# Optimization experiments

Hardware: AMD Instinct MI355X
Metric: run time of the kernel (lower is better)

Reference implementation:

```python
import jax, jax.numpy as jnp
import numpy as np

N, E, D = 50000, 300000, 64
EPS = 0.0  # eps buffer, train_eps=False


def setup_inputs() -> dict:
    key = jax.random.key(0)
    ks = jax.random.split(key, 24)
    inp = {}
    i = 0
    for d in range(3):
        inp[f"x{d}"] = jax.random.normal(ks[i], (N, D), jnp.float32); i += 1
        inp[f"up_index{d}"] = jax.random.randint(ks[i], (2, E), 0, N, jnp.int32); i += 1
        inp[f"down_index{d}"] = jax.random.randint(ks[i], (2, E), 0, N, jnp.int32); i += 1
        inp[f"up_attr{d}"] = jax.random.normal(ks[i], (E, D), jnp.float32); i += 1
        inp[f"down_attr{d}"] = jax.random.normal(ks[i], (E, D), jnp.float32); i += 1
    s2 = 1.0 / np.sqrt(2 * D)
    s1 = 1.0 / np.sqrt(D)
    inp["W_up"] = jax.random.normal(ks[i], (2 * D, D), jnp.float32) * s2; i += 1
    inp["b_up"] = jnp.zeros((D,), jnp.float32)
    inp["W_down"] = jax.random.normal(ks[i], (2 * D, D), jnp.float32) * s2; i += 1
    inp["b_down"] = jnp.zeros((D,), jnp.float32)
    inp["W1"] = jax.random.normal(ks[i], (D, D), jnp.float32) * s1; i += 1
    inp["b1"] = jnp.zeros((D,), jnp.float32)
    inp["W2"] = jax.random.normal(ks[i], (D, D), jnp.float32) * s1; i += 1
    inp["b2"] = jnp.zeros((D,), jnp.float32)
    return inp


def _level(x, up_idx, down_idx, up_attr, down_attr,
           W_up, b_up, W_down, b_down, W1, b1, W2, b2):
    # message_up: gather source feats, concat attr, MLP, scatter-add to targets
    m_up = jax.nn.relu(jnp.concatenate([x[up_idx[1]], up_attr], axis=-1) @ W_up + b_up)
    out_up = jax.ops.segment_sum(m_up, up_idx[0], num_segments=N)
    m_dn = jax.nn.relu(jnp.concatenate([x[down_idx[1]], down_attr], axis=-1) @ W_down + b_down)
    out_dn = jax.ops.segment_sum(m_dn, down_idx[0], num_segments=N)
    # out_up += (1+eps)x; out_down += (1+eps)x; update(out_up + out_down)
    h = out_up + out_dn + (2.0 * (1.0 + EPS)) * x
    return jax.nn.relu(jax.nn.relu(h @ W1 + b1) @ W2 + b2)


def reference(x0, up_index0, down_index0, up_attr0, down_attr0,
              x1, up_index1, down_index1, up_attr1, down_attr1,
              x2, up_index2, down_index2, up_attr2, down_attr2,
              W_up, b_up, W_down, b_down, W1, b1, W2, b2):
    params = (W_up, b_up, W_down, b_down, W1, b1, W2, b2)
    o0 = _level(x0, up_index0, down_index0, up_attr0, down_attr0, *params)
    o1 = _level(x1, up_index1, down_index1, up_attr1, down_attr1, *params)
    o2 = _level(x2, up_index2, down_index2, up_attr2, down_attr2, *params)
    return (o0, o1, o2)
```

## Files before the change

### kernel.cpp

```cpp
#include <hip/hip_runtime.h>
#include <hip/hip_fp16.h>

#define NN 50000
#define NE 300000
#define ETILES (NE / 16)
#define NTILES (NN / 16)

typedef _Float16 f16;
typedef _Float16 f16x4 __attribute__((ext_vector_type(4)));
typedef _Float16 f16x8 __attribute__((ext_vector_type(8)));
typedef float f32x4 __attribute__((ext_vector_type(4)));

__device__ __forceinline__ f16x4 cvt4(float4 v) {
    f16x4 r; r.x = (f16)v.x; r.y = (f16)v.y; r.z = (f16)v.z; r.w = (f16)v.w;
    return r;
}

__global__ void init2_kernel(const float* __restrict__ x0, const float* __restrict__ x1,
                             const float* __restrict__ x2,
                             f16* __restrict__ hbase, f16* __restrict__ xhbase) {
    const size_t i = (size_t)blockIdx.x * 256 + threadIdx.x;
    const int lvl = (int)(i / (NN * 16));
    const size_t li = i - (size_t)lvl * (NN * 16);
    const float* xs = (lvl == 0) ? x0 : (lvl == 1) ? x1 : x2;
    float4 v = ((const float4*)xs)[li];
    f16x4 xo, ho;
    xo.x = (f16)v.x;        xo.y = (f16)v.y;        xo.z = (f16)v.z;        xo.w = (f16)v.w;
    ho.x = (f16)(2.f*v.x);  ho.y = (f16)(2.f*v.y);  ho.z = (f16)(2.f*v.z);  ho.w = (f16)(2.f*v.w);
    ((f16x4*)(xhbase + (size_t)lvl * NN * 64))[li] = xo;
    ((f16x4*)(hbase  + (size_t)lvl * NN * 64))[li] = ho;
}

__global__ void initf32_kernel(const float* __restrict__ x0, const float* __restrict__ x1,
                               const float* __restrict__ x2, float* __restrict__ hbase) {
    const size_t i = (size_t)blockIdx.x * 256 + threadIdx.x;
    const int lvl = (int)(i / (NN * 16));
    const size_t li = i - (size_t)lvl * (NN * 16);
    const float* xs = (lvl == 0) ? x0 : (lvl == 1) ? x1 : x2;
    float4 v = ((const float4*)xs)[li];
    ((float4*)(hbase + (size_t)lvl * NN * 64))[li] =
        make_float4(2.f * v.x, 2.f * v.y, 2.f * v.z, 2.f * v.w);
}

__global__ void wtrans_kernel(const float* __restrict__ WU, const float* __restrict__ WD,
                              f16* __restrict__ WtU, f16* __restrict__ WtD) {
    const int i = blockIdx.x * 256 + threadIdx.x;
    const int k = i >> 6, c = i & 63;
    WtU[c * 128 + k] = (f16)WU[i];
    WtD[c * 128 + k] = (f16)WD[i];
}

#define WLDS_STRIDE 136

__device__ __forceinline__ int ld_comb(const int* __restrict__ idx, int tile, int l5) {
    const int e0 = tile << 4;
    return idx[(l5 < 16) ? (NE + e0 + l5) : (e0 + l5 - 16)];
}

__global__ __launch_bounds__(256) void edge4_kernel(
    const f16* __restrict__ xh,
    const int* __restrict__ ui, const int* __restrict__ di,
    const float* __restrict__ ua, const float* __restrict__ da,
    const f16* __restrict__ WtU, const f16* __restrict__ WtD,
    const float* __restrict__ bU, const float* __restrict__ bD,
    __half* __restrict__ h) {

    __shared__ __align__(16) f16 Wlds[64 * WLDS_STRIDE];

    const int dir = blockIdx.y;
    const int* __restrict__ idx    = dir ? di : ui;
    const float* __restrict__ attr = dir ? da : ua;
    const f16* __restrict__ Wt     = dir ? WtD : WtU;
    const float* __restrict__ b    = dir ? bD : bU;

    const int tt   = threadIdx.x;
    const int lane = tt & 63;
    const int wid  = tt >> 6;
    const int lr   = lane & 15;
    const int lg   = (lane >> 4) & 3;
    const int l5   = lane & 31;

    for (int i = tt; i < 1024; i += 256) {
        const int row = i >> 4, seg = i & 15;
        *(f16x8*)&Wlds[row * WLDS_STRIDE + seg * 8] = *(const f16x8*)&Wt[row * 128 + seg * 8];
    }
    float bf[4];
#pragma unroll
    for (int n = 0; n < 4; ++n) bf[n] = b[n * 16 + lr];
    __syncthreads();

    const float4* a4 = (const float4*)attr;

    const int S = gridDim.x * 4;
    int t = blockIdx.x * 4 + wid;
    if (t >= ETILES) return;

    int cB;
    int srcT, tgT[4];
    f16x4 gx[4];
    float4 pA[4];
    {
        const int cA = ld_comb(idx, t, l5);
        const int tn1 = t + S;
        cB = ld_comb(idx, (tn1 < ETILES) ? tn1 : t, l5);
        srcT = __shfl(cA, lr);
#pragma unroll
        for (int j = 0; j < 4; ++j) tgT[j] = __shfl(cA, 16 + 4 * lg + j);
        const int e0 = t << 4;
#pragma unroll
        for (int k0 = 0; k0 < 4; ++k0)
            gx[k0] = *(const f16x4*)&xh[(size_t)srcT * 64 + k0 * 16 + 4 * lg];
#pragma unroll
        for (int k0 = 0; k0 < 4; ++k0)
            pA[k0] = a4[(size_t)(e0 + lr) * 16 + 4 * k0 + lg];
    }

    for (; t < ETILES; t += S) {
        const int tn  = t + S;
        const int tnn = tn + S;

        const int srcN = __shfl(cB, lr);
        int tgN[4];
#pragma unroll
        for (int j = 0; j < 4; ++j) tgN[j] = __shfl(cB, 16 + 4 * lg + j);
        const int cC = ld_comb(idx, (tnn < ETILES) ? tnn : t, l5);

        const int tnc   = (tn < ETILES) ? tn : t;
        const int srcNc = (tn < ETILES) ? srcN : srcT;
        f16x4 gxN[4];
        float4 pAN[4];
        {
            const int e0n = tnc << 4;
#pragma unroll
            for (int k0 = 0; k0 < 4; ++k0)
                gxN[k0] = *(const f16x4*)&xh[(size_t)srcNc * 64 + k0 * 16 + 4 * lg];
#pragma unroll
            for (int k0 = 0; k0 < 4; ++k0)
                pAN[k0] = a4[(size_t)(e0n + lr) * 16 + 4 * k0 + lg];
        }

        f16x4 afr[8];
#pragma unroll
        for (int k0 = 0; k0 < 4; ++k0) afr[k0] = gx[k0];
#pragma unroll
        for (int k0 = 0; k0 < 4; ++k0) afr[4 + k0] = cvt4(pA[k0]);

        f32x4 acc[4];
#pragma unroll
        for (int n = 0; n < 4; ++n) acc[n] = (f32x4){0.f, 0.f, 0.f, 0.f};
#pragma unroll
        for (int k0 = 0; k0 < 8; ++k0) {
#pragma unroll
            for (int n = 0; n < 4; ++n) {
                const f16x4 wf = *(const f16x4*)&Wlds[(n * 16 + lr) * WLDS_STRIDE + k0 * 16 + 4 * lg];
                acc[n] = __builtin_amdgcn_mfma_f32_16x16x16f16(afr[k0], wf, acc[n], 0, 0, 0);
            }
        }

#pragma unroll
        for (int j = 0; j < 4; ++j) {
            float v[4], vn[4];
#pragma unroll
            for (int n = 0; n < 4; ++n) v[n] = fmaxf(acc[n][j] + bf[n], 0.f);
#pragma unroll
            for (int n = 0; n < 4; ++n) vn[n] = __shfl_xor(v[n], 1);
            __half* hp = h + (size_t)tgT[j] * 64;
            if ((lane & 1) == 0) {
                unsafeAtomicAdd((__half2*)(hp + 0 * 16 + lr), __floats2half2_rn(v[0], vn[0]));
                unsafeAtomicAdd((__half2*)(hp + 1 * 16 + lr), __floats2half2_rn(v[1], vn[1]));
            } else {
                unsafeAtomicAdd((__half2*)(hp + 2 * 16 + lr - 1), __floats2half2_rn(vn[2], v[2]));
                unsafeAtomicAdd((__half2*)(hp + 3 * 16 + lr - 1), __floats2half2_rn(vn[3], v[3]));
            }
        }

        srcT = srcN;
#pragma unroll
        for (int j = 0; j < 4; ++j) tgT[j] = tgN[j];
#pragma unroll
        for (int k0 = 0; k0 < 4; ++k0) { gx[k0] = gxN[k0]; pA[k0] = pAN[k0]; }
        cB = cC;
    }
}

__global__ __launch_bounds__(256) void edge_f32_kernel(
    const float* __restrict__ x, const int* __restrict__ idx,
    const float* __restrict__ attr, const float* __restrict__ W,
    const float* __restrict__ b, float* __restrict__ h) {

    const int t    = threadIdx.x;
    const int lane = t & 63;
    const int wid  = t >> 6;
    const int lr   = lane & 15;
    const int lg   = (lane >> 4) & 3;

    f16x4 wf[8][4];
#pragma unroll
    for (int k0 = 0; k0 < 8; ++k0) {
        const int kb = k0 * 16 + 4 * lg;
#pragma unroll
        for (int n = 0; n < 4; ++n) {
            const int c = n * 16 + lr;
            f16x4 w;
            w.x = (f16)W[(kb + 0) * 64 + c];
            w.y = (f16)W[(kb + 1) * 64 + c];
            w.z = (f16)W[(kb + 2) * 64 + c];
            w.w = (f16)W[(kb + 3) * 64 + c];
            wf[k0][n] = w;
        }
    }
    float bf[4];
#pragma unroll
    for (int n = 0; n < 4; ++n) bf[n] = b[n * 16 + lr];

    const float4* x4 = (const float4*)x;
    const float4* a4 = (const float4*)attr;

    const int gw     = blockIdx.x * 4 + wid;
    const int stride = gridDim.x * 4;
    for (int tile = gw; tile < ETILES; tile += stride) {
        const int e0  = tile << 4;
        const int src = idx[NE + e0 + lr];
        int tg[4];
#pragma unroll
        for (int j = 0; j < 4; ++j) tg[j] = idx[e0 + 4 * lg + j];

        f16x4 a[8];
#pragma unroll
        for (int k0 = 0; k0 < 4; ++k0)
            a[k0] = cvt4(x4[(size_t)src * 16 + 4 * k0 + lg]);
#pragma unroll
        for (int k0 = 0; k0 < 4; ++k0)
            a[4 + k0] = cvt4(a4[(size_t)(e0 + lr) * 16 + 4 * k0 + lg]);

        f32x4 acc[4];
#pragma unroll
        for (int n = 0; n < 4; ++n) acc[n] = (f32x4){0.f, 0.f, 0.f, 0.f};
#pragma unroll
        for (int k0 = 0; k0 < 8; ++k0)
#pragma unroll
            for (int n = 0; n < 4; ++n)
                acc[n] = __builtin_amdgcn_mfma_f32_16x16x16f16(a[k0], wf[k0][n], acc[n], 0, 0, 0);

#pragma unroll
        for (int j = 0; j < 4; ++j) {
            float* hp = h + (size_t)tg[j] * 64;
#pragma unroll
            for (int n = 0; n < 4; ++n) {
                float v = fmaxf(acc[n][j] + bf[n], 0.f);
                unsafeAtomicAdd(hp + n * 16 + lr, v);
            }
        }
    }
}

template<bool HALF>
__global__ __launch_bounds__(256) void node_kernel(
    const void* __restrict__ hbase, float* __restrict__ outb,
    const float* __restrict__ W1, const float* __restrict__ b1,
    const float* __restrict__ W2, const float* __restrict__ b2) {

    __shared__ f16 Y[4][16 * 72];

    const int t    = threadIdx.x;
    const int lane = t & 63;
    const int wid  = t >> 6;
    const int lr   = lane & 15;
    const int lg   = (lane >> 4) & 3;

    f16x4 w1f[4][4], w2f[4][4];
#pragma unroll
    for (int k0 = 0; k0 < 4; ++k0) {
        const int kb = k0 * 16 + 4 * lg;
#pragma unroll
        for (int n = 0; n < 4; ++n) {
            const int c = n * 16 + lr;
            f16x4 w;
            w.x = (f16)W1[(kb + 0) * 64 + c];
            w.y = (f16)W1[(kb + 1) * 64 + c];
            w.z = (f16)W1[(kb + 2) * 64 + c];
            w.w = (f16)W1[(kb + 3) * 64 + c];
            w1f[k0][n] = w;
            w.x = (f16)W2[(kb + 0) * 64 + c];
            w.y = (f16)W2[(kb + 1) * 64 + c];
            w.z = (f16)W2[(kb + 2) * 64 + c];
            w.w = (f16)W2[(kb + 3) * 64 + c];
            w2f[k0][n] = w;
        }
    }
    float b1f[4], b2f[4];
#pragma unroll
    for (int n = 0; n < 4; ++n) {
        b1f[n] = b1[n * 16 + lr];
        b2f[n] = b2[n * 16 + lr];
    }

    const int gw     = blockIdx.x * 4 + wid;
    const int stride = gridDim.x * 4;
    for (int tile = gw; tile < 3 * NTILES; tile += stride) {
        const int lvl = tile / NTILES;
        const int n0  = (tile - lvl * NTILES) << 4;
        float* out = outb + (size_t)lvl * NN * 64;

        f16x4 a[4];
        if (HALF) {
            const f16* h16 = (const f16*)hbase + (size_t)lvl * NN * 64;
#pragma unroll
            for (int k0 = 0; k0 < 4; ++k0)
                a[k0] = *(const f16x4*)&h16[(size_t)(n0 + lr) * 64 + k0 * 16 + 4 * lg];
        } else {
            const float4* h4 = (const float4*)((const float*)hbase + (size_t)lvl * NN * 64);
#pragma unroll
            for (int k0 = 0; k0 < 4; ++k0)
                a[k0] = cvt4(h4[(size_t)(n0 + lr) * 16 + 4 * k0 + lg]);
        }

        f32x4 acc[4];
#pragma unroll
        for (int n = 0; n < 4; ++n) acc[n] = (f32x4){0.f, 0.f, 0.f, 0.f};
#pragma unroll
        for (int k0 = 0; k0 < 4; ++k0)
#pragma unroll
            for (int n = 0; n < 4; ++n)
                acc[n] = __builtin_amdgcn_mfma_f32_16x16x16f16(a[k0], w1f[k0][n], acc[n], 0, 0, 0);

#pragma unroll
        for (int n = 0; n < 4; ++n)
#pragma unroll
            for (int j = 0; j < 4; ++j) {
                float v = acc[n][j] + b1f[n];
                v = v > 0.f ? v : 0.f;
                Y[wid][(4 * lg + j) * 72 + n * 16 + lr] = (f16)v;
            }

        f16x4 a2[4];
#pragma unroll
        for (int k0 = 0; k0 < 4; ++k0)
            a2[k0] = *(const f16x4*)&Y[wid][lr * 72 + k0 * 16 + 4 * lg];

        f32x4 acc2[4];
#pragma unroll
        for (int n = 0; n < 4; ++n) acc2[n] = (f32x4){0.f, 0.f, 0.f, 0.f};
#pragma unroll
        for (int k0 = 0; k0 < 4; ++k0)
#pragma unroll
            for (int n = 0; n < 4; ++n)
                acc2[n] = __builtin_amdgcn_mfma_f32_16x16x16f16(a2[k0], w2f[k0][n], acc2[n], 0, 0, 0);

#pragma unroll
        for (int n = 0; n < 4; ++n)
#pragma unroll
            for (int j = 0; j < 4; ++j) {
                float v = acc2[n][j] + b2f[n];
                v = v > 0.f ? v : 0.f;
                out[(size_t)(n0 + 4 * lg + j) * 64 + n * 16 + lr] = v;
            }
    }
}

extern "C" void kernel_launch(void* const* d_in, const int* in_sizes, int n_in,
                              void* d_out, int out_size, void* d_ws, size_t ws_size,
                              hipStream_t stream) {
    (void)in_sizes; (void)n_in; (void)out_size;

    const float* W_up   = (const float*)d_in[15];
    const float* b_up   = (const float*)d_in[16];
    const float* W_down = (const float*)d_in[17];
    const float* b_down = (const float*)d_in[18];
    const float* W1     = (const float*)d_in[19];
    const float* b1     = (const float*)d_in[20];
    const float* W2     = (const float*)d_in[21];
    const float* b2     = (const float*)d_in[22];

    const float* x0 = (const float*)d_in[0];
    const float* x1 = (const float*)d_in[5];
    const float* x2 = (const float*)d_in[10];

    const size_t hbytes  = (size_t)3 * NN * 64 * sizeof(f16);
    const size_t need    = 2 * hbytes + (size_t)2 * 128 * 64 * sizeof(f16);

    if (ws_size >= need) {
        f16* hbase  = (f16*)d_ws;
        f16* xhbase = hbase + (size_t)3 * NN * 64;
        f16* WtU    = (f16*)((char*)d_ws + 2 * hbytes);
        f16* WtD    = WtU + 128 * 64;

        wtrans_kernel<<<32, 256, 0, stream>>>(W_up, W_down, WtU, WtD);
        init2_kernel<<<9375, 256, 0, stream>>>(x0, x1, x2, hbase, xhbase);
        for (int d = 0; d < 3; ++d) {
            const int*   ui = (const int*)  d_in[5 * d + 1];
            const int*   di = (const int*)  d_in[5 * d + 2];
            const float* ua = (const float*)d_in[5 * d + 3];
            const float* da = (const float*)d_in[5 * d + 4];
            const f16* xh = xhbase + (size_t)d * NN * 64;
            __half* h = (__half*)(hbase + (size_t)d * NN * 64);
            edge4_kernel<<<dim3(1024, 2), 256, 0, stream>>>(
                xh, ui, di, ua, da, WtU, WtD, b_up, b_down, h);
        }
        node_kernel<true><<<586, 256, 0, stream>>>(hbase, (float*)d_out, W1, b1, W2, b2);
    } else {
        float* hbase = (float*)d_out;
        initf32_kernel<<<9375, 256, 0, stream>>>(x0, x1, x2, hbase);
        for (int d = 0; d < 3; ++d) {
            const float* x  = (const float*)d_in[5 * d + 0];
            const int*   ui = (const int*)  d_in[5 * d + 1];
            const int*   di = (const int*)  d_in[5 * d + 2];
            const float* ua = (const float*)d_in[5 * d + 3];
            const float* da = (const float*)d_in[5 * d + 4];
            float* h = hbase + (size_t)d * NN * 64;
            edge_f32_kernel<<<1024, 256, 0, stream>>>(x, ui, ua, W_up,   b_up,   h);
            edge_f32_kernel<<<1024, 256, 0, stream>>>(x, di, da, W_down, b_down, h);
        }
        node_kernel<false><<<586, 256, 0, stream>>>(hbase, (float*)d_out, W1, b1, W2, b2);
    }
}
```

Before: 433.8 us.

## Replace fp16 atomic scatter with CSR sort-by-target and deterministic segment aggregation

Builds a CSR layout per edge set on device: a histogram of targets, a three-pass prefix scan, and a scatter that gives each edge a slot. The edge MLP kernel then writes fp16 messages to their sorted slot instead of doing fp16 atomic adds. An aggregation kernel sums each node's contiguous messages plus 2x in fp32. This removes contended half2 atomics and accumulates in fp32, but adds about ten small kernel launches, atomics in the histogram and scatter passes, and a large message buffer written and read back. The old software-pipelined edge kernel is simplified and kept only as a fallback when the workspace is too small.

```diff
diff --git a/kernel.cpp b/kernel.cpp
--- a/kernel.cpp
+++ b/kernel.cpp
@@ -5,11 +5,14 @@
 #define NE 300000
 #define ETILES (NE / 16)
 #define NTILES (NN / 16)
+#define WLDS_STRIDE 136
 
 typedef _Float16 f16;
 typedef _Float16 f16x4 __attribute__((ext_vector_type(4)));
 typedef _Float16 f16x8 __attribute__((ext_vector_type(8)));
 typedef float f32x4 __attribute__((ext_vector_type(4)));
+
+struct Idx6 { const int* p[6]; };
 
 __device__ __forceinline__ f16x4 cvt4(float4 v) {
     f16x4 r; r.x = (f16)v.x; r.y = (f16)v.y; r.z = (f16)v.z; r.w = (f16)v.w;
@@ -31,17 +34,6 @@
     ((f16x4*)(hbase  + (size_t)lvl * NN * 64))[li] = ho;
 }
 
-__global__ void initf32_kernel(const float* __restrict__ x0, const float* __restrict__ x1,
-                               const float* __restrict__ x2, float* __restrict__ hbase) {
-    const size_t i = (size_t)blockIdx.x * 256 + threadIdx.x;
-    const int lvl = (int)(i / (NN * 16));
-    const size_t li = i - (size_t)lvl * (NN * 16);
-    const float* xs = (lvl == 0) ? x0 : (lvl == 1) ? x1 : x2;
-    float4 v = ((const float4*)xs)[li];
-    ((float4*)(hbase + (size_t)lvl * NN * 64))[li] =
-        make_float4(2.f * v.x, 2.f * v.y, 2.f * v.z, 2.f * v.w);
-}
-
 __global__ void wtrans_kernel(const float* __restrict__ WU, const float* __restrict__ WD,
                               f16* __restrict__ WtU, f16* __restrict__ WtD) {
     const int i = blockIdx.x * 256 + threadIdx.x;
@@ -50,7 +42,179 @@
     WtD[c * 128 + k] = (f16)WD[i];
 }
 
-#define WLDS_STRIDE 136
+__global__ void zero_cnt_kernel(int* __restrict__ cnt) {
+    const int i = blockIdx.x * 256 + threadIdx.x;
+    if (i < 6 * NN) cnt[i] = 0;
+}
+
+__global__ void hist_kernel(Idx6 idx, int* __restrict__ cnt) {
+    const int e = blockIdx.x * 256 + threadIdx.x;
+    const int d = blockIdx.y;
+    if (e < NE) atomicAdd(&cnt[d * NN + idx.p[d][e]], 1);
+}
+
+__device__ __forceinline__ int block_incl_scan(int v, int tid, int* sb) {
+    sb[tid] = v; __syncthreads();
+#pragma unroll
+    for (int off = 1; off < 256; off <<= 1) {
+        int t = (tid >= off) ? sb[tid - off] : 0;
+        __syncthreads();
+        sb[tid] += t;
+        __syncthreads();
+    }
+    return sb[tid];
+}
+
+__global__ void scan1_kernel(const int* __restrict__ cnt, int* __restrict__ rptmp,
+                             int* __restrict__ bsum) {
+    __shared__ int sb[256];
+    const int d = blockIdx.y, tid = threadIdx.x;
+    const int i = blockIdx.x * 256 + tid;
+    const int v = (i < NN) ? cnt[d * NN + i] : 0;
+    const int incl = block_incl_scan(v, tid, sb);
+    if (i < NN) rptmp[d * NN + i] = incl - v;
+    if (tid == 255) bsum[d * 256 + blockIdx.x] = incl;
+}
+
+__global__ void scan2_kernel(int* __restrict__ bsum) {
+    __shared__ int sb[256];
+    const int d = blockIdx.x, tid = threadIdx.x;
+    const int v = (tid < 196) ? bsum[d * 256 + tid] : 0;
+    const int incl = block_incl_scan(v, tid, sb);
+    bsum[d * 256 + tid] = incl - v;
+}
+
+__global__ void scan3_kernel(const int* __restrict__ cnt, const int* __restrict__ rptmp,
+                             const int* __restrict__ bsum,
+                             int* __restrict__ rowptr, int* __restrict__ cursor) {
+    const int d = blockIdx.y;
+    const int i = blockIdx.x * 256 + threadIdx.x;
+    if (i < NN) {
+        const int v = rptmp[d * NN + i] + bsum[d * 256 + blockIdx.x];
+        rowptr[d * (NN + 1) + i] = v;
+        cursor[d * NN + i] = v;
+        if (i == NN - 1) rowptr[d * (NN + 1) + NN] = v + cnt[d * NN + i];
+    }
+}
+
+__global__ void scatter_kernel(Idx6 idx, int* __restrict__ cursor, int* __restrict__ pos) {
+    const int e = blockIdx.x * 256 + threadIdx.x;
+    const int d = blockIdx.y;
+    if (e < NE) pos[(size_t)d * NE + e] = atomicAdd(&cursor[d * NN + idx.p[d][e]], 1);
+}
+
+__global__ __launch_bounds__(256) void edge_mlp_kernel(
+    const f16* __restrict__ xh,
+    const int* __restrict__ ui, const int* __restrict__ di,
+    const float* __restrict__ ua, const float* __restrict__ da,
+    const f16* __restrict__ WtU, const f16* __restrict__ WtD,
+    const float* __restrict__ bU, const float* __restrict__ bD,
+    const int* __restrict__ posU, const int* __restrict__ posD,
+    __half* __restrict__ mU, __half* __restrict__ mD) {
+
+    __shared__ __align__(16) f16 Wlds[64 * WLDS_STRIDE];
+
+    const int dir = blockIdx.y;
+    const int* __restrict__ idx    = dir ? di : ui;
+    const float* __restrict__ attr = dir ? da : ua;
+    const f16* __restrict__ Wt     = dir ? WtD : WtU;
+    const float* __restrict__ b    = dir ? bD : bU;
+    const int* __restrict__ pos    = dir ? posD : posU;
+    __half* __restrict__ m         = dir ? mD : mU;
+
+    const int tt   = threadIdx.x;
+    const int lane = tt & 63;
+    const int wid  = tt >> 6;
+    const int lr   = lane & 15;
+    const int lg   = (lane >> 4) & 3;
+
+    for (int i = tt; i < 1024; i += 256) {
+        const int row = i >> 4, seg = i & 15;
+        *(f16x8*)&Wlds[row * WLDS_STRIDE + seg * 8] = *(const f16x8*)&Wt[row * 128 + seg * 8];
+    }
+    float bf[4];
+#pragma unroll
+    for (int n = 0; n < 4; ++n) bf[n] = b[n * 16 + lr];
+    __syncthreads();
+
+    const int tile = blockIdx.x * 4 + wid;
+    if (tile >= ETILES) return;
+    const int e0 = tile << 4;
+
+    const int src = idx[NE + e0 + lr];
+    const int pv  = pos[e0 + lr];
+
+    const float4* a4 = (const float4*)attr;
+
+    f16x4 afr[8];
+#pragma unroll
+    for (int k0 = 0; k0 < 4; ++k0)
+        afr[k0] = *(const f16x4*)&xh[(size_t)src * 64 + k0 * 16 + 4 * lg];
+#pragma unroll
+    for (int k0 = 0; k0 < 4; ++k0)
+        afr[4 + k0] = cvt4(a4[(size_t)(e0 + lr) * 16 + 4 * k0 + lg]);
+
+    f32x4 acc[4];
+#pragma unroll
+    for (int n = 0; n < 4; ++n) acc[n] = (f32x4){0.f, 0.f, 0.f, 0.f};
+#pragma unroll
+    for (int k0 = 0; k0 < 8; ++k0) {
+#pragma unroll
+        for (int n = 0; n < 4; ++n) {
+            const f16x4 wf = *(const f16x4*)&Wlds[(n * 16 + lr) * WLDS_STRIDE + k0 * 16 + 4 * lg];
+            acc[n] = __builtin_amdgcn_mfma_f32_16x16x16f16(afr[k0], wf, acc[n], 0, 0, 0);
+        }
+    }
+
+#pragma unroll
+    for (int j = 0; j < 4; ++j) {
+        float v[4], vn[4];
+#pragma unroll
+        for (int n = 0; n < 4; ++n) v[n] = fmaxf(acc[n][j] + bf[n], 0.f);
+#pragma unroll
+        for (int n = 0; n < 4; ++n) vn[n] = __shfl_xor(v[n], 1);
+        const int s = __shfl(pv, 4 * lg + j);
+        __half* mp = m + (size_t)s * 64;
+        if ((lane & 1) == 0) {
+            *(__half2*)(mp + 0 * 16 + lr) = __floats2half2_rn(v[0], vn[0]);
+            *(__half2*)(mp + 1 * 16 + lr) = __floats2half2_rn(v[1], vn[1]);
+        } else {
+            *(__half2*)(mp + 2 * 16 + lr - 1) = __floats2half2_rn(vn[2], v[2]);
+            *(__half2*)(mp + 3 * 16 + lr - 1) = __floats2half2_rn(vn[3], v[3]);
+        }
+    }
+}
+
+__global__ __launch_bounds__(256) void agg_kernel(
+    const float* __restrict__ x,
+    const __half* __restrict__ mU, const __half* __restrict__ mD,
+    const int* __restrict__ rpU, const int* __restrict__ rpD,
+    f16* __restrict__ agg) {
+
+    const int tid  = threadIdx.x;
+    const int node = blockIdx.x * 16 + (tid >> 4);
+    const int c4   = tid & 15;
+
+    float4 xv = ((const float4*)x)[(size_t)node * 16 + c4];
+    float a0 = 2.f * xv.x, a1 = 2.f * xv.y, a2 = 2.f * xv.z, a3 = 2.f * xv.w;
+
+    {
+        const int beg = rpU[node], end = rpU[node + 1];
+        for (int k = beg; k < end; ++k) {
+            f16x4 mv = *(const f16x4*)((const f16*)mU + (size_t)k * 64 + c4 * 4);
+            a0 += (float)mv.x; a1 += (float)mv.y; a2 += (float)mv.z; a3 += (float)mv.w;
+        }
+    }
+    {
+        const int beg = rpD[node], end = rpD[node + 1];
+        for (int k = beg; k < end; ++k) {
+            f16x4 mv = *(const f16x4*)((const f16*)mD + (size_t)k * 64 + c4 * 4);
+            a0 += (float)mv.x; a1 += (float)mv.y; a2 += (float)mv.z; a3 += (float)mv.w;
+        }
+    }
+    f16x4 o; o.x = (f16)a0; o.y = (f16)a1; o.z = (f16)a2; o.w = (f16)a3;
+    *(f16x4*)&agg[(size_t)node * 64 + c4 * 4] = o;
+}
 
 __device__ __forceinline__ int ld_comb(const int* __restrict__ idx, int tile, int l5) {
     const int e0 = tile << 4;
@@ -90,72 +254,36 @@
     __syncthreads();
 
     const float4* a4 = (const float4*)attr;
-
     const int S = gridDim.x * 4;
     int t = blockIdx.x * 4 + wid;
     if (t >= ETILES) return;
 
-    int cB;
-    int srcT, tgT[4];
-    f16x4 gx[4];
-    float4 pA[4];
-    {
+    for (; t < ETILES; t += S) {
+        const int e0 = t << 4;
         const int cA = ld_comb(idx, t, l5);
-        const int tn1 = t + S;
-        cB = ld_comb(idx, (tn1 < ETILES) ? tn1 : t, l5);
-        srcT = __shfl(cA, lr);
-#pragma unroll
-        for (int j = 0; j < 4; ++j) tgT[j] = __shfl(cA, 16 + 4 * lg + j);
-        const int e0 = t << 4;
-#pragma unroll
-        for (int k0 = 0; k0 < 4; ++k0)
-            gx[k0] = *(const f16x4*)&xh[(size_t)srcT * 64 + k0 * 16 + 4 * lg];
-#pragma unroll
-        for (int k0 = 0; k0 < 4; ++k0)
-            pA[k0] = a4[(size_t)(e0 + lr) * 16 + 4 * k0 + lg];
-    }
-
-    for (; t < ETILES; t += S) {
-        const int tn  = t + S;
-        const int tnn = tn + S;
-
-        const int srcN = __shfl(cB, lr);
-        int tgN[4];
-#pragma unroll
-        for (int j = 0; j < 4; ++j) tgN[j] = __shfl(cB, 16 + 4 * lg + j);
-        const int cC = ld_comb(idx, (tnn < ETILES) ? tnn : t, l5);
-
-        const int tnc   = (tn < ETILES) ? tn : t;
-        const int srcNc = (tn < ETILES) ? srcN : srcT;
-        f16x4 gxN[4];
-        float4 pAN[4];
-        {
-            const int e0n = tnc << 4;
-#pragma unroll
-            for (int k0 = 0; k0 < 4; ++k0)
-                gxN[k0] = *(const f16x4*)&xh[(size_t)srcNc * 64 + k0 * 16 + 4 * lg];
-#pragma unroll
-            for (int k0 = 0; k0 < 4; ++k0)
-                pAN[k0] = a4[(size_t)(e0n + lr) * 16 + 4 * k0 + lg];
-        }
+        const int src = __shfl(cA, lr);
+        int tg[4];
+#pragma unroll
+        for (int j = 0; j < 4; ++j) tg[j] = __shfl(cA, 16 + 4 * lg + j);
 
         f16x4 afr[8];
 #pragma unroll
-        for (int k0 = 0; k0 < 4; ++k0) afr[k0] = gx[k0];
-#pragma unroll
-        for (int k0 = 0; k0 < 4; ++k0) afr[4 + k0] = cvt4(pA[k0]);
+        for (int k0 = 0; k0 < 4; ++k0)
+            afr[k0] = *(const f16x4*)&xh[(size_t)src * 64 + k0 * 16 + 4 * lg];
+#pragma unroll
+        for (int k0 = 0; k0 < 4; ++k0)
+            afr[4 + k0] = cvt4(a4[(size_t)(e0 + lr) * 16 + 4 * k0 + lg]);
 
         f32x4 acc[4];
 #pragma unroll
         for (int n = 0; n < 4; ++n) acc[n] = (f32x4){0.f, 0.f, 0.f, 0.f};
 #pragma unroll
-        for (int k0 = 0; k0 < 8; ++k0) {
+        for (int k0 = 0; k0 < 8; ++k0)
 #pragma unroll
             for (int n = 0; n < 4; ++n) {
                 const f16x4 wf = *(const f16x4*)&Wlds[(n * 16 + lr) * WLDS_STRIDE + k0 * 16 + 4 * lg];
                 acc[n] = __builtin_amdgcn_mfma_f32_16x16x16f16(afr[k0], wf, acc[n], 0, 0, 0);
             }
-        }
 
 #pragma unroll
         for (int j = 0; j < 4; ++j) {
@@ -164,7 +292,7 @@
             for (int n = 0; n < 4; ++n) v[n] = fmaxf(acc[n][j] + bf[n], 0.f);
 #pragma unroll
             for (int n = 0; n < 4; ++n) vn[n] = __shfl_xor(v[n], 1);
-            __half* hp = h + (size_t)tgT[j] * 64;
+            __half* hp = h + (size_t)tg[j] * 64;
             if ((lane & 1) == 0) {
                 unsafeAtomicAdd((__half2*)(hp + 0 * 16 + lr), __floats2half2_rn(v[0], vn[0]));
                 unsafeAtomicAdd((__half2*)(hp + 1 * 16 + lr), __floats2half2_rn(v[1], vn[1]));
@@ -173,90 +301,11 @@
                 unsafeAtomicAdd((__half2*)(hp + 3 * 16 + lr - 1), __floats2half2_rn(vn[3], v[3]));
             }
         }
-
-        srcT = srcN;
-#pragma unroll
-        for (int j = 0; j < 4; ++j) tgT[j] = tgN[j];
-#pragma unroll
-        for (int k0 = 0; k0 < 4; ++k0) { gx[k0] = gxN[k0]; pA[k0] = pAN[k0]; }
-        cB = cC;
-    }
-}
-
-__global__ __launch_bounds__(256) void edge_f32_kernel(
-    const float* __restrict__ x, const int* __restrict__ idx,
-    const float* __restrict__ attr, const float* __restrict__ W,
-    const float* __restrict__ b, float* __restrict__ h) {
-
-    const int t    = threadIdx.x;
-    const int lane = t & 63;
-    const int wid  = t >> 6;
-    const int lr   = lane & 15;
-    const int lg   = (lane >> 4) & 3;
-
-    f16x4 wf[8][4];
-#pragma unroll
-    for (int k0 = 0; k0 < 8; ++k0) {
-        const int kb = k0 * 16 + 4 * lg;
-#pragma unroll
-        for (int n = 0; n < 4; ++n) {
-            const int c = n * 16 + lr;
-            f16x4 w;
-            w.x = (f16)W[(kb + 0) * 64 + c];
-            w.y = (f16)W[(kb + 1) * 64 + c];
-            w.z = (f16)W[(kb + 2) * 64 + c];
-            w.w = (f16)W[(kb + 3) * 64 + c];
-            wf[k0][n] = w;
-        }
-    }
-    float bf[4];
-#pragma unroll
-    for (int n = 0; n < 4; ++n) bf[n] = b[n * 16 + lr];
-
-    const float4* x4 = (const float4*)x;
-    const float4* a4 = (const float4*)attr;
-
-    const int gw     = blockIdx.x * 4 + wid;
-    const int stride = gridDim.x * 4;
-    for (int tile = gw; tile < ETILES; tile += stride) {
-        const int e0  = tile << 4;
-        const int src = idx[NE + e0 + lr];
-        int tg[4];
-#pragma unroll
-        for (int j = 0; j < 4; ++j) tg[j] = idx[e0 + 4 * lg + j];
-
-        f16x4 a[8];
-#pragma unroll
-        for (int k0 = 0; k0 < 4; ++k0)
-            a[k0] = cvt4(x4[(size_t)src * 16 + 4 * k0 + lg]);
-#pragma unroll
-        for (int k0 = 0; k0 < 4; ++k0)
-            a[4 + k0] = cvt4(a4[(size_t)(e0 + lr) * 16 + 4 * k0 + lg]);
-
-        f32x4 acc[4];
-#pragma unroll
-        for (int n = 0; n < 4; ++n) acc[n] = (f32x4){0.f, 0.f, 0.f, 0.f};
-#pragma unroll
-        for (int k0 = 0; k0 < 8; ++k0)
-#pragma unroll
-            for (int n = 0; n < 4; ++n)
-                acc[n] = __builtin_amdgcn_mfma_f32_16x16x16f16(a[k0], wf[k0][n], acc[n], 0, 0, 0);
-
-#pragma unroll
-        for (int j = 0; j < 4; ++j) {
-            float* hp = h + (size_t)tg[j] * 64;
-#pragma unroll
-            for (int n = 0; n < 4; ++n) {
-                float v = fmaxf(acc[n][j] + bf[n], 0.f);
-                unsafeAtomicAdd(hp + n * 16 + lr, v);
-            }
-        }
-    }
-}
-
-template<bool HALF>
+    }
+}
+
 __global__ __launch_bounds__(256) void node_kernel(
-    const void* __restrict__ hbase, float* __restrict__ outb,
+    const f16* __restrict__ hbase, float* __restrict__ outb,
     const float* __restrict__ W1, const float* __restrict__ b1,
     const float* __restrict__ W2, const float* __restrict__ b2) {
 
@@ -301,19 +350,12 @@
         const int lvl = tile / NTILES;
         const int n0  = (tile - lvl * NTILES) << 4;
         float* out = outb + (size_t)lvl * NN * 64;
+        const f16* h16 = hbase + (size_t)lvl * NN * 64;
 
         f16x4 a[4];
-        if (HALF) {
-            const f16* h16 = (const f16*)hbase + (size_t)lvl * NN * 64;
-#pragma unroll
-            for (int k0 = 0; k0 < 4; ++k0)
-                a[k0] = *(const f16x4*)&h16[(size_t)(n0 + lr) * 64 + k0 * 16 + 4 * lg];
-        } else {
-            const float4* h4 = (const float4*)((const float*)hbase + (size_t)lvl * NN * 64);
-#pragma unroll
-            for (int k0 = 0; k0 < 4; ++k0)
-                a[k0] = cvt4(h4[(size_t)(n0 + lr) * 16 + 4 * k0 + lg]);
-        }
+#pragma unroll
+        for (int k0 = 0; k0 < 4; ++k0)
+            a[k0] = *(const f16x4*)&h16[(size_t)(n0 + lr) * 64 + k0 * 16 + 4 * lg];
 
         f32x4 acc[4];
 #pragma unroll
@@ -376,41 +418,82 @@
     const float* x1 = (const float*)d_in[5];
     const float* x2 = (const float*)d_in[10];
 
-    const size_t hbytes  = (size_t)3 * NN * 64 * sizeof(f16);
-    const size_t need    = 2 * hbytes + (size_t)2 * 128 * 64 * sizeof(f16);
-
-    if (ws_size >= need) {
-        f16* hbase  = (f16*)d_ws;
-        f16* xhbase = hbase + (size_t)3 * NN * 64;
-        f16* WtU    = (f16*)((char*)d_ws + 2 * hbytes);
-        f16* WtD    = WtU + 128 * 64;
+    size_t off = 0;
+    auto alloc = [&](size_t bytes) { size_t o = off; off = (off + bytes + 255) & ~(size_t)255; return o; };
+    const size_t o_xh   = alloc((size_t)3 * NN * 64 * 2);
+    const size_t o_agg  = alloc((size_t)3 * NN * 64 * 2);
+    const size_t o_wt   = alloc((size_t)2 * 128 * 64 * 2);
+    const size_t fallback_need = off;
+    const size_t o_m    = alloc((size_t)2 * NE * 64 * 2);
+    const size_t o_pos  = alloc((size_t)6 * NE * 4);
+    const size_t o_rp   = alloc((size_t)6 * (NN + 1) * 4);
+    const size_t o_cur  = alloc((size_t)6 * NN * 4);
+    const size_t o_rpt  = alloc((size_t)6 * NN * 4);
+    const size_t o_bsum = alloc((size_t)6 * 256 * 4);
+    const size_t o_cnt  = alloc((size_t)6 * NN * 4);
+    const size_t full_need = off;
+
+    char* ws = (char*)d_ws;
+    f16*  xh   = (f16*)(ws + o_xh);
+    f16*  agg  = (f16*)(ws + o_agg);
+    f16*  WtU  = (f16*)(ws + o_wt);
+    f16*  WtD  = WtU + 128 * 64;
+
+    if (ws_size >= full_need) {
+        __half* mU  = (__half*)(ws + o_m);
+        __half* mD  = mU + (size_t)NE * 64;
+        int* pos    = (int*)(ws + o_pos);
+        int* rowptr = (int*)(ws + o_rp);
+        int* cursor = (int*)(ws + o_cur);
+        int* rptmp  = (int*)(ws + o_rpt);
+        int* bsum   = (int*)(ws + o_bsum);
+        int* cnt    = (int*)(ws + o_cnt);
+
+        Idx6 idx;
+        for (int d = 0; d < 3; ++d) {
+            idx.p[2 * d + 0] = (const int*)d_in[5 * d + 1];
+            idx.p[2 * d + 1] = (const int*)d_in[5 * d + 2];
+        }
+
+        zero_cnt_kernel<<<1172, 256, 0, stream>>>(cnt);
+        hist_kernel<<<dim3(1172, 6), 256, 0, stream>>>(idx, cnt);
+        scan1_kernel<<<dim3(196, 6), 256, 0, stream>>>(cnt, rptmp, bsum);
+        scan2_kernel<<<6, 256, 0, stream>>>(bsum);
+        scan3_kernel<<<dim3(196, 6), 256, 0, stream>>>(cnt, rptmp, bsum, rowptr, cursor);
+        scatter_kernel<<<dim3(1172, 6), 256, 0, stream>>>(idx, cursor, pos);
 
         wtrans_kernel<<<32, 256, 0, stream>>>(W_up, W_down, WtU, WtD);
-        init2_kernel<<<9375, 256, 0, stream>>>(x0, x1, x2, hbase, xhbase);
-        for (int d = 0; d < 3; ++d) {
-            const int*   ui = (const int*)  d_in[5 * d + 1];
-            const int*   di = (const int*)  d_in[5 * d + 2];
-            const float* ua = (const float*)d_in[5 * d + 3];
-            const float* da = (const float*)d_in[5 * d + 4];
-            const f16* xh = xhbase + (size_t)d * NN * 64;
-            __half* h = (__half*)(hbase + (size_t)d * NN * 64);
-            edge4_kernel<<<dim3(1024, 2), 256, 0, stream>>>(
-                xh, ui, di, ua, da, WtU, WtD, b_up, b_down, h);
-        }
-        node_kernel<true><<<586, 256, 0, stream>>>(hbase, (float*)d_out, W1, b1, W2, b2);
-    } else {
-        float* hbase = (float*)d_out;
-        initf32_kernel<<<9375, 256, 0, stream>>>(x0, x1, x2, hbase);
+        init2_kernel<<<9375, 256, 0, stream>>>(x0, x1, x2, agg, xh);
+
         for (int d = 0; d < 3; ++d) {
             const float* x  = (const float*)d_in[5 * d + 0];
             const int*   ui = (const int*)  d_in[5 * d + 1];
             const int*   di = (const int*)  d_in[5 * d + 2];
             const float* ua = (const float*)d_in[5 * d + 3];
             const float* da = (const float*)d_in[5 * d + 4];
-            float* h = hbase + (size_t)d * NN * 64;
-            edge_f32_kernel<<<1024, 256, 0, stream>>>(x, ui, ua, W_up,   b_up,   h);
-            edge_f32_kernel<<<1024, 256, 0, stream>>>(x, di, da, W_down, b_down, h);
-        }
-        node_kernel<false><<<586, 256, 0, stream>>>(hbase, (float*)d_out, W1, b1, W2, b2);
-    }
-}
+            const f16* xhd = xh + (size_t)d * NN * 64;
+            edge_mlp_kernel<<<dim3(4688, 2), 256, 0, stream>>>(
+                xhd, ui, di, ua, da, WtU, WtD, b_up, b_down,
+                pos + (size_t)(2 * d) * NE, pos + (size_t)(2 * d + 1) * NE, mU, mD);
+            agg_kernel<<<3125, 256, 0, stream>>>(
+                x, mU, mD,
+                rowptr + (size_t)(2 * d) * (NN + 1), rowptr + (size_t)(2 * d + 1) * (NN + 1),
+                agg + (size_t)d * NN * 64);
+        }
+        node_kernel<<<586, 256, 0, stream>>>(agg, (float*)d_out, W1, b1, W2, b2);
+    } else if (ws_size >= fallback_need) {
+        wtrans_kernel<<<32, 256, 0, stream>>>(W_up, W_down, WtU, WtD);
+        init2_kernel<<<9375, 256, 0, stream>>>(x0, x1, x2, agg, xh);
+        for (int d = 0; d < 3; ++d) {
+            const int*   ui = (const int*)  d_in[5 * d + 1];
+            const int*   di = (const int*)  d_in[5 * d + 2];
+            const float* ua = (const float*)d_in[5 * d + 3];
+            const float* da = (const float*)d_in[5 * d + 4];
+            const f16* xhd = xh + (size_t)d * NN * 64;
+            __half* h = (__half*)(agg + (size_t)d * NN * 64);
+            edge4_kernel<<<dim3(1024, 2), 256, 0, stream>>>(
+                xhd, ui, di, ua, da, WtU, WtD, b_up, b_down, h);
+        }
+        node_kernel<<<586, 256, 0, stream>>>(agg, (float*)d_out, W1, b1, W2, b2);
+    }
+}
```

After: 476.0 us. 1.1x slower.
